# Kernel tuning notes

Hardware: AMD Instinct MI355X
Metric: run time of the kernel (lower is better)

## Reference

```python
import jax, jax.numpy as jnp
import numpy as np

B, S, D_IN, D_OUT, H = 2, 2048, 1024, 1024, 16
HD = D_OUT // H

def setup_inputs() -> dict:
    key = jax.random.key(0)
    ks = jax.random.split(key, 6)
    sc_in = 1.0 / np.sqrt(D_IN)
    sc_out = 1.0 / np.sqrt(D_OUT)
    return {
        "x": jax.random.normal(ks[0], (B, S, D_IN), dtype=jnp.float32),
        "Wq": jax.random.uniform(ks[1], (D_IN, D_OUT), jnp.float32, -sc_in, sc_in),
        "Wk": jax.random.uniform(ks[2], (D_IN, D_OUT), jnp.float32, -sc_in, sc_in),
        "Wv": jax.random.uniform(ks[3], (D_IN, D_OUT), jnp.float32, -sc_in, sc_in),
        "Wo": jax.random.uniform(ks[4], (D_OUT, D_OUT), jnp.float32, -sc_out, sc_out),
        "bo": jax.random.uniform(ks[5], (D_OUT,), jnp.float32, -sc_out, sc_out),
    }

def reference(x, Wq, Wk, Wv, Wo, bo):
    b, s, _ = x.shape
    # QKV projections (no bias), split heads -> [b, h, s, hd]
    q = (x @ Wq).reshape(b, s, H, HD).transpose(0, 2, 1, 3)
    k = (x @ Wk).reshape(b, s, H, HD).transpose(0, 2, 1, 3)
    v = (x @ Wv).reshape(b, s, H, HD).transpose(0, 2, 1, 3)
    scores = jnp.einsum('bhqd,bhkd->bhqk', q, k)
    causal = jnp.triu(jnp.ones((s, s), dtype=bool), k=1)
    scores = jnp.where(causal, -jnp.inf, scores)
    w = jax.nn.softmax(scores / np.sqrt(HD), axis=-1)  # dropout p=0.0 -> identity
    ctx = jnp.einsum('bhqk,bhkd->bhqd', w, v)
    ctx = ctx.transpose(0, 2, 1, 3).reshape(b, s, D_OUT)
    return ctx @ Wo + bo
```

## Files before the change

### kernel.cpp

```cpp
#include <hip/hip_runtime.h>
#include <stdint.h>

typedef unsigned short u16;
typedef __attribute__((ext_vector_type(8))) short short8;
typedef __attribute__((ext_vector_type(4))) float floatx4;
typedef __attribute__((ext_vector_type(4))) u16 ushort4v;

typedef __attribute__((address_space(1))) const uint32_t gu32;
typedef __attribute__((address_space(3))) uint32_t lu32;

#define MFMA(a, b, c) __builtin_amdgcn_mfma_f32_16x16x32_bf16((a), (b), (c), 0, 0, 0)

__device__ __forceinline__ u16 f2bf(float f) {
    union { float f; uint32_t u; } x; x.f = f;
    uint32_t u = x.u;
    u += 0x7fffu + ((u >> 16) & 1u);
    return (u16)(u >> 16);
}

__device__ __forceinline__ void async16(u16* lds, const u16* g) {
    __builtin_amdgcn_global_load_lds((gu32*)g, (lu32*)lds, 16, 0, 0);
}

__global__ __launch_bounds__(256) void prep_kernel(
    const float* __restrict__ x,
    const float* __restrict__ W0, const float* __restrict__ W1,
    const float* __restrict__ W2, const float* __restrict__ W3,
    u16* __restrict__ WT, u16* __restrict__ Xbf)
{
    const int z = blockIdx.z;
    const int tx = threadIdx.x, ty = threadIdx.y;
    if (z == 4) {
        const int bid = blockIdx.y * 32 + blockIdx.x;
        const int t = ty * 32 + tx;
        const size_t base = ((size_t)bid * 256 + t) * 16;
        const float* xf = x + base;
        short8 v0, v1;
#pragma unroll
        for (int j = 0; j < 8; j++) v0[j] = (short)f2bf(xf[j]);
#pragma unroll
        for (int j = 0; j < 8; j++) v1[j] = (short)f2bf(xf[8 + j]);
        *(short8*)&Xbf[base] = v0;
        *(short8*)&Xbf[base + 8] = v1;
        return;
    }
    __shared__ u16 tile[32][33];
    const float* W = (z == 0) ? W0 : (z == 1) ? W1 : (z == 2) ? W2 : W3;
    u16* dst = WT + (size_t)z * 1024 * 1024;
    const int n0 = blockIdx.x * 32, k0 = blockIdx.y * 32;
#pragma unroll
    for (int i = 0; i < 4; i++)
        tile[ty + i * 8][tx] = f2bf(W[(size_t)(k0 + ty + i * 8) * 1024 + n0 + tx]);
    __syncthreads();
#pragma unroll
    for (int i = 0; i < 4; i++)
        dst[(size_t)(n0 + ty + i * 8) * 1024 + k0 + tx] = tile[tx][ty + i * 8];
}

__global__ __launch_bounds__(256) void gemm_qkv_kernel(
    const u16* __restrict__ X, const u16* __restrict__ WT,
    u16* __restrict__ Q, u16* __restrict__ Kout, u16* __restrict__ VT)
{
    __shared__ __align__(16) u16 As[128 * 32];
    __shared__ __align__(16) u16 Bs[128 * 32];
    const int bid = blockIdx.x;
    const int xcd = bid & 7;
    const int idx = bid >> 3;
    const int mat = idx >> 5;
    const int rr  = (idx >> 3) & 3;
    const int nn  = idx & 7;
    const int m0 = (xcd * 4 + rr) * 128;
    const int n0 = nn * 128;
    const u16* BW = WT + (size_t)mat * 1024 * 1024;
    const int tid = threadIdx.x;
    const int wave = tid >> 6, lane = tid & 63;
    const int lrow = lane & 15, lquad = lane >> 4;
    const int wr = (wave >> 1) * 64, wc = (wave & 1) * 64;

    const int ci0 = wave * 128 + lane;
    const int ci1 = ci0 + 64;
    const int ar0 = ci0 >> 2, ac0 = (ci0 & 3) * 8;
    const int ar1 = ci1 >> 2, ac1 = (ci1 & 3) * 8;
    u16* ldsA0 = As + (size_t)(wave * 128) * 8;
    u16* ldsA1 = As + (size_t)(wave * 128 + 64) * 8;
    u16* ldsB0 = Bs + (size_t)(wave * 128) * 8;
    u16* ldsB1 = Bs + (size_t)(wave * 128 + 64) * 8;
    const u16* gA0 = &X[(size_t)(m0 + ar0) * 1024 + ac0];
    const u16* gA1 = &X[(size_t)(m0 + ar1) * 1024 + ac1];
    const u16* gB0 = &BW[(size_t)(n0 + ar0) * 1024 + ac0];
    const u16* gB1 = &BW[(size_t)(n0 + ar1) * 1024 + ac1];

    floatx4 acc[4][4];
#pragma unroll
    for (int mt = 0; mt < 4; mt++)
#pragma unroll
        for (int nt = 0; nt < 4; nt++) acc[mt][nt] = (floatx4){0.f, 0.f, 0.f, 0.f};

    for (int k0 = 0; k0 < 1024; k0 += 32) {
        __syncthreads();
        async16(ldsA0, gA0 + k0);
        async16(ldsA1, gA1 + k0);
        async16(ldsB0, gB0 + k0);
        async16(ldsB1, gB1 + k0);
        __syncthreads();
        short8 af[4], bf[4];
#pragma unroll
        for (int mt = 0; mt < 4; mt++)
            af[mt] = *(const short8*)&As[(wr + mt * 16 + lrow) * 32 + lquad * 8];
#pragma unroll
        for (int nt = 0; nt < 4; nt++)
            bf[nt] = *(const short8*)&Bs[(wc + nt * 16 + lrow) * 32 + lquad * 8];
#pragma unroll
        for (int mt = 0; mt < 4; mt++)
#pragma unroll
            for (int nt = 0; nt < 4; nt++)
                acc[mt][nt] = MFMA(af[mt], bf[nt], acc[mt][nt]);
    }

#pragma unroll
    for (int mt = 0; mt < 4; mt++) {
        const int gm = m0 + wr + mt * 16 + lquad * 4;
        const int b_ = gm >> 11;
        const int s  = gm & 2047;
#pragma unroll
        for (int nt = 0; nt < 4; nt++) {
            const int gn = n0 + wc + nt * 16 + lrow;
            const int h = gn >> 6, hd = gn & 63;
            const int bh = b_ * 16 + h;
            if (mat == 2) {
                ushort4v v;
#pragma unroll
                for (int i = 0; i < 4; i++) v[i] = f2bf(acc[mt][nt][i]);
                *(ushort4v*)&VT[((size_t)bh * 64 + hd) * 2048 + s] = v;
            } else {
                u16* dst = (mat == 0) ? Q : Kout;
#pragma unroll
                for (int i = 0; i < 4; i++)
                    dst[((size_t)bh * 2048 + s + i) * 64 + hd] = f2bf(acc[mt][nt][i]);
            }
        }
    }
}

__global__ __launch_bounds__(256, 4) void attn_kernel(
    const u16* __restrict__ Q, const u16* __restrict__ Kk,
    const u16* __restrict__ VT, u16* __restrict__ ctx)
{
    __shared__ __align__(16) u16 Ks[64][72];
    __shared__ __align__(16) u16 Vs[64][72];
    __shared__ __align__(16) u16 P[4][16][72];
    const int tid = threadIdx.x, wave = tid >> 6, lane = tid & 63;
    const int lrow = lane & 15, lquad = lane >> 4;
    const float scale = 0.125f;
    const float NEGINF = -__builtin_inff();

    const int bh = blockIdx.x & 31;
    const int g = blockIdx.x >> 5;
    const int qb = (g < 16) ? (31 - g) : (g - 16);
    const int ntiles = qb + 1;
    const int q0 = qb * 64 + wave * 16;

    const u16* Qb = Q  + (size_t)bh * 2048 * 64;
    const u16* Kb = Kk + (size_t)bh * 2048 * 64;
    const u16* Vb = VT + (size_t)bh * 64 * 2048;

    const short8 qf0 = *(const short8*)&Qb[(size_t)(q0 + lrow) * 64 + lquad * 8];
    const short8 qf1 = *(const short8*)&Qb[(size_t)(q0 + lrow) * 64 + 32 + lquad * 8];

    const int myq = q0 + lrow;
    float m_s = NEGINF, l_s = 0.f;
    floatx4 o[4];
#pragma unroll
    for (int i = 0; i < 4; i++) o[i] = (floatx4){0.f, 0.f, 0.f, 0.f};

    const int r0 = tid >> 3, c0 = (tid & 7) * 8;
    const int r1 = (tid + 256) >> 3, c1 = c0;

    short8 kreg0 = *(const short8*)&Kb[(size_t)r0 * 64 + c0];
    short8 kreg1 = *(const short8*)&Kb[(size_t)r1 * 64 + c1];
    short8 vreg0 = *(const short8*)&Vb[(size_t)r0 * 2048 + c0];
    short8 vreg1 = *(const short8*)&Vb[(size_t)r1 * 2048 + c1];

    for (int kt = 0; kt < ntiles; kt++) {
        __syncthreads();
        *(short8*)&Ks[r0][c0] = kreg0;
        *(short8*)&Ks[r1][c1] = kreg1;
        *(short8*)&Vs[r0][c0] = vreg0;
        *(short8*)&Vs[r1][c1] = vreg1;
        if (kt + 1 < ntiles) {
            kreg0 = *(const short8*)&Kb[(size_t)((kt + 1) * 64 + r0) * 64 + c0];
            kreg1 = *(const short8*)&Kb[(size_t)((kt + 1) * 64 + r1) * 64 + c1];
            vreg0 = *(const short8*)&Vb[(size_t)r0 * 2048 + (kt + 1) * 64 + c0];
            vreg1 = *(const short8*)&Vb[(size_t)r1 * 2048 + (kt + 1) * 64 + c1];
        }
        __syncthreads();

        floatx4 s[4];
#pragma unroll
        for (int nt = 0; nt < 4; nt++) {
            const short8 kf0 = *(const short8*)&Ks[nt * 16 + lrow][lquad * 8];
            const short8 kf1 = *(const short8*)&Ks[nt * 16 + lrow][32 + lquad * 8];
            floatx4 a = (floatx4){0.f, 0.f, 0.f, 0.f};
            a = MFMA(kf0, qf0, a);
            a = MFMA(kf1, qf1, a);
            s[nt] = a;
        }

        const bool diag = (kt == ntiles - 1);
        float mx = NEGINF;
#pragma unroll
        for (int nt = 0; nt < 4; nt++)
#pragma unroll
            for (int i = 0; i < 4; i++) {
                float v = s[nt][i] * scale;
                if (diag && (kt * 64 + nt * 16 + lquad * 4 + i > myq)) v = NEGINF;
                s[nt][i] = v;
                mx = fmaxf(mx, v);
            }
        mx = fmaxf(mx, __shfl_xor(mx, 16));
        mx = fmaxf(mx, __shfl_xor(mx, 32));
        const float mnew = fmaxf(m_s, mx);
        const float alpha = __expf(m_s - mnew);
        m_s = mnew;
        float sum = 0.f;
#pragma unroll
        for (int nt = 0; nt < 4; nt++)
#pragma unroll
            for (int i = 0; i < 4; i++) {
                const float pv = __expf(s[nt][i] - mnew);
                s[nt][i] = pv;
                sum += pv;
            }
        sum += __shfl_xor(sum, 16);
        sum += __shfl_xor(sum, 32);
        l_s = l_s * alpha + sum;
#pragma unroll
        for (int ht = 0; ht < 4; ht++)
#pragma unroll
            for (int i = 0; i < 4; i++) o[ht][i] *= alpha;

#pragma unroll
        for (int nt = 0; nt < 4; nt++) {
            uint32_t pk0 = (uint32_t)f2bf(s[nt][0]) | ((uint32_t)f2bf(s[nt][1]) << 16);
            uint32_t pk1 = (uint32_t)f2bf(s[nt][2]) | ((uint32_t)f2bf(s[nt][3]) << 16);
            uint2 pk = {pk0, pk1};
            *(uint2*)&P[wave][lrow][nt * 16 + lquad * 4] = pk;
        }
#pragma unroll
        for (int st = 0; st < 2; st++) {
            const short8 pf = *(const short8*)&P[wave][lrow][st * 32 + lquad * 8];
#pragma unroll
            for (int ht = 0; ht < 4; ht++) {
                const short8 vf = *(const short8*)&Vs[ht * 16 + lrow][st * 32 + lquad * 8];
                o[ht] = MFMA(vf, pf, o[ht]);
            }
        }
    }

    const int b_ = bh >> 4, h_ = bh & 15;
    const float inv_l = 1.0f / l_s;
#pragma unroll
    for (int ht = 0; ht < 4; ht++) {
        uint32_t pk0 = (uint32_t)f2bf(o[ht][0] * inv_l) | ((uint32_t)f2bf(o[ht][1] * inv_l) << 16);
        uint32_t pk1 = (uint32_t)f2bf(o[ht][2] * inv_l) | ((uint32_t)f2bf(o[ht][3] * inv_l) << 16);
        uint2 pk = {pk0, pk1};
        *(uint2*)&ctx[((size_t)(b_ * 2048 + q0 + lrow)) * 1024 + h_ * 64 + ht * 16 + lquad * 4] = pk;
    }
}

__global__ __launch_bounds__(256) void gemm_out_kernel(
    const u16* __restrict__ X, const u16* __restrict__ WT,
    const float* __restrict__ bias, float* __restrict__ out)
{
    __shared__ __align__(16) u16 As[128 * 32];
    __shared__ __align__(16) u16 Bs[128 * 32];
    const int bid = blockIdx.x;
    const int xcd = bid & 7;
    const int idx = bid >> 3;
    const int rr  = idx >> 3;
    const int nn  = idx & 7;
    const int m0 = (xcd * 4 + rr) * 128;
    const int n0 = nn * 128;
    const int tid = threadIdx.x;
    const int wave = tid >> 6, lane = tid & 63;
    const int lrow = lane & 15, lquad = lane >> 4;
    const int wr = (wave >> 1) * 64, wc = (wave & 1) * 64;

    const int ci0 = wave * 128 + lane;
    const int ci1 = ci0 + 64;
    const int ar0 = ci0 >> 2, ac0 = (ci0 & 3) * 8;
    const int ar1 = ci1 >> 2, ac1 = (ci1 & 3) * 8;
    u16* ldsA0 = As + (size_t)(wave * 128) * 8;
    u16* ldsA1 = As + (size_t)(wave * 128 + 64) * 8;
    u16* ldsB0 = Bs + (size_t)(wave * 128) * 8;
    u16* ldsB1 = Bs + (size_t)(wave * 128 + 64) * 8;
    const u16* gA0 = &X[(size_t)(m0 + ar0) * 1024 + ac0];
    const u16* gA1 = &X[(size_t)(m0 + ar1) * 1024 + ac1];
    const u16* gB0 = &WT[(size_t)(n0 + ar0) * 1024 + ac0];
    const u16* gB1 = &WT[(size_t)(n0 + ar1) * 1024 + ac1];

    floatx4 acc[4][4];
#pragma unroll
    for (int mt = 0; mt < 4; mt++)
#pragma unroll
        for (int nt = 0; nt < 4; nt++) acc[mt][nt] = (floatx4){0.f, 0.f, 0.f, 0.f};

    for (int k0 = 0; k0 < 1024; k0 += 32) {
        __syncthreads();
        async16(ldsA0, gA0 + k0);
        async16(ldsA1, gA1 + k0);
        async16(ldsB0, gB0 + k0);
        async16(ldsB1, gB1 + k0);
        __syncthreads();
        short8 af[4], bf[4];
#pragma unroll
        for (int mt = 0; mt < 4; mt++)
            af[mt] = *(const short8*)&As[(wr + mt * 16 + lrow) * 32 + lquad * 8];
#pragma unroll
        for (int nt = 0; nt < 4; nt++)
            bf[nt] = *(const short8*)&Bs[(wc + nt * 16 + lrow) * 32 + lquad * 8];
#pragma unroll
        for (int mt = 0; mt < 4; mt++)
#pragma unroll
            for (int nt = 0; nt < 4; nt++)
                acc[mt][nt] = MFMA(af[mt], bf[nt], acc[mt][nt]);
    }

#pragma unroll
    for (int mt = 0; mt < 4; mt++) {
        const int gm = m0 + wr + mt * 16 + lquad * 4;
#pragma unroll
        for (int nt = 0; nt < 4; nt++) {
            const int gn = n0 + wc + nt * 16 + lrow;
            const float bv = bias[gn];
#pragma unroll
            for (int i = 0; i < 4; i++)
                out[(size_t)(gm + i) * 1024 + gn] = acc[mt][nt][i] + bv;
        }
    }
}

extern "C" void kernel_launch(void* const* d_in, const int* in_sizes, int n_in,
                              void* d_out, int out_size, void* d_ws, size_t ws_size,
                              hipStream_t stream) {
    u16* ws = (u16*)d_ws + 64;

    const size_t MB1 = 1024 * 1024;
    u16* WT   = ws;
    u16* Qw   = ws + 4 * MB1;
    u16* Kw   = ws + 8 * MB1;
    u16* VTw  = ws + 12 * MB1;
    u16* ctxw = ws + 16 * MB1;
    u16* Xbf  = ws + 20 * MB1;

    prep_kernel<<<dim3(32, 32, 5), dim3(32, 8), 0, stream>>>(
        (const float*)d_in[0], (const float*)d_in[1], (const float*)d_in[2],
        (const float*)d_in[3], (const float*)d_in[4], WT, Xbf);
    gemm_qkv_kernel<<<768, 256, 0, stream>>>(Xbf, WT, Qw, Kw, VTw);
    attn_kernel<<<1024, 256, 0, stream>>>(Qw, Kw, VTw, ctxw);
    gemm_out_kernel<<<256, 256, 0, stream>>>(ctxw, WT + 3 * MB1, (const float*)d_in[5], (float*)d_out);
}
```

Baseline: 181.6 us.

## Double-buffer K/V via async LDS loads with swizzled tile layout and exp2 softmax

The QKV GEMM epilogue now writes K and V in per-64-row tiles with an XOR swizzle, so the attention kernel can copy each tile straight into LDS with global_load_lds. K/V tiles are double-buffered, which removes the register staging and one barrier per iteration. Q is pre-scaled by scale*log2e so the softmax can use exp2 without a per-element multiply. P is packed to bf16 by truncation. The risks are correctness of the async-load waits under a single barrier, and the slightly different rounding of P.

```diff
diff --git a/kernel.cpp b/kernel.cpp
--- a/kernel.cpp
+++ b/kernel.cpp
@@ -10,12 +10,18 @@
 typedef __attribute__((address_space(3))) uint32_t lu32;
 
 #define MFMA(a, b, c) __builtin_amdgcn_mfma_f32_16x16x32_bf16((a), (b), (c), 0, 0, 0)
+
+#define QSCALE 0.1803368801111204f
 
 __device__ __forceinline__ u16 f2bf(float f) {
     union { float f; uint32_t u; } x; x.f = f;
     uint32_t u = x.u;
     u += 0x7fffu + ((u >> 16) & 1u);
     return (u16)(u >> 16);
+}
+
+__device__ __forceinline__ uint32_t pack_trunc(float hi, float lo) {
+    return __builtin_amdgcn_perm(__float_as_uint(hi), __float_as_uint(lo), 0x07060302u);
 }
 
 __device__ __forceinline__ void async16(u16* lds, const u16* g) {
@@ -122,36 +128,45 @@
         const int gm = m0 + wr + mt * 16 + lquad * 4;
         const int b_ = gm >> 11;
         const int s  = gm & 2047;
+        const int kt = s >> 6;
+        const int r  = s & 63;
 #pragma unroll
         for (int nt = 0; nt < 4; nt++) {
             const int gn = n0 + wc + nt * 16 + lrow;
             const int h = gn >> 6, hd = gn & 63;
             const int bh = b_ * 16 + h;
             if (mat == 2) {
+                const size_t base = ((size_t)(bh * 32 + kt) * 64 + hd) * 64
+                                  + ((((r >> 3) ^ (hd & 7)) << 3) | (r & 7));
                 ushort4v v;
 #pragma unroll
                 for (int i = 0; i < 4; i++) v[i] = f2bf(acc[mt][nt][i]);
-                *(ushort4v*)&VT[((size_t)bh * 64 + hd) * 2048 + s] = v;
+                *(ushort4v*)&VT[base] = v;
+            } else if (mat == 1) {
+#pragma unroll
+                for (int i = 0; i < 4; i++) {
+                    const int r2 = r + i;
+                    Kout[((size_t)(bh * 32 + kt) * 64 + r2) * 64
+                         + (((hd >> 3) ^ (r2 & 7)) << 3) + (hd & 7)] = f2bf(acc[mt][nt][i]);
+                }
             } else {
-                u16* dst = (mat == 0) ? Q : Kout;
 #pragma unroll
                 for (int i = 0; i < 4; i++)
-                    dst[((size_t)bh * 2048 + s + i) * 64 + hd] = f2bf(acc[mt][nt][i]);
+                    Q[((size_t)bh * 2048 + s + i) * 64 + hd] = f2bf(acc[mt][nt][i] * QSCALE);
             }
         }
     }
 }
 
 __global__ __launch_bounds__(256, 4) void attn_kernel(
-    const u16* __restrict__ Q, const u16* __restrict__ Kk,
-    const u16* __restrict__ VT, u16* __restrict__ ctx)
+    const u16* __restrict__ Q, const u16* __restrict__ Ksw,
+    const u16* __restrict__ Vsw, u16* __restrict__ ctx)
 {
-    __shared__ __align__(16) u16 Ks[64][72];
-    __shared__ __align__(16) u16 Vs[64][72];
-    __shared__ __align__(16) u16 P[4][16][72];
+    __shared__ __align__(16) u16 Ks[2][4096];
+    __shared__ __align__(16) u16 Vs[2][4096];
+    __shared__ __align__(16) u16 P[4][1024];
     const int tid = threadIdx.x, wave = tid >> 6, lane = tid & 63;
     const int lrow = lane & 15, lquad = lane >> 4;
-    const float scale = 0.125f;
     const float NEGINF = -__builtin_inff();
 
     const int bh = blockIdx.x & 31;
@@ -160,12 +175,35 @@
     const int ntiles = qb + 1;
     const int q0 = qb * 64 + wave * 16;
 
-    const u16* Qb = Q  + (size_t)bh * 2048 * 64;
-    const u16* Kb = Kk + (size_t)bh * 2048 * 64;
-    const u16* Vb = VT + (size_t)bh * 64 * 2048;
+    const u16* Qb = Q   + (size_t)bh * 2048 * 64;
+    const u16* Kt = Ksw + (size_t)bh * 32 * 4096;
+    const u16* Vt = Vsw + (size_t)bh * 32 * 4096;
 
     const short8 qf0 = *(const short8*)&Qb[(size_t)(q0 + lrow) * 64 + lquad * 8];
     const short8 qf1 = *(const short8*)&Qb[(size_t)(q0 + lrow) * 64 + 32 + lquad * 8];
+
+    const int r7 = lrow & 7;
+    int koff0[4], koff1[4], voff[2][4];
+#pragma unroll
+    for (int nt = 0; nt < 4; nt++) {
+        const int row = nt * 16 + lrow;
+        koff0[nt] = row * 64 + ((lquad ^ r7) << 3);
+        koff1[nt] = row * 64 + (((4 + lquad) ^ r7) << 3);
+    }
+#pragma unroll
+    for (int st = 0; st < 2; st++)
+#pragma unroll
+        for (int ht = 0; ht < 4; ht++) {
+            const int row = ht * 16 + lrow;
+            voff[st][ht] = row * 64 + (((st * 4 + lquad) ^ r7) << 3);
+        }
+    int pwoff[4], proff[2];
+#pragma unroll
+    for (int nt = 0; nt < 4; nt++)
+        pwoff[nt] = lrow * 64 + (((nt * 2 + (lquad >> 1)) ^ r7) << 3) + ((lquad & 1) << 2);
+#pragma unroll
+    for (int st = 0; st < 2; st++)
+        proff[st] = lrow * 64 + (((st * 4 + lquad) ^ r7) << 3);
 
     const int myq = q0 + lrow;
     float m_s = NEGINF, l_s = 0.f;
@@ -173,33 +211,36 @@
 #pragma unroll
     for (int i = 0; i < 4; i++) o[i] = (floatx4){0.f, 0.f, 0.f, 0.f};
 
-    const int r0 = tid >> 3, c0 = (tid & 7) * 8;
-    const int r1 = (tid + 256) >> 3, c1 = c0;
-
-    short8 kreg0 = *(const short8*)&Kb[(size_t)r0 * 64 + c0];
-    short8 kreg1 = *(const short8*)&Kb[(size_t)r1 * 64 + c1];
-    short8 vreg0 = *(const short8*)&Vb[(size_t)r0 * 2048 + c0];
-    short8 vreg1 = *(const short8*)&Vb[(size_t)r1 * 2048 + c1];
+    const int co0 = wave * 1024;
+    const int co1 = wave * 1024 + 512;
+    const int lo8 = lane * 8;
+
+    async16(&Ks[0][co0], Kt + co0 + lo8);
+    async16(&Ks[0][co1], Kt + co1 + lo8);
+    async16(&Vs[0][co0], Vt + co0 + lo8);
+    async16(&Vs[0][co1], Vt + co1 + lo8);
+
+    u16* Pw = P[wave];
 
     for (int kt = 0; kt < ntiles; kt++) {
         __syncthreads();
-        *(short8*)&Ks[r0][c0] = kreg0;
-        *(short8*)&Ks[r1][c1] = kreg1;
-        *(short8*)&Vs[r0][c0] = vreg0;
-        *(short8*)&Vs[r1][c1] = vreg1;
         if (kt + 1 < ntiles) {
-            kreg0 = *(const short8*)&Kb[(size_t)((kt + 1) * 64 + r0) * 64 + c0];
-            kreg1 = *(const short8*)&Kb[(size_t)((kt + 1) * 64 + r1) * 64 + c1];
-            vreg0 = *(const short8*)&Vb[(size_t)r0 * 2048 + (kt + 1) * 64 + c0];
-            vreg1 = *(const short8*)&Vb[(size_t)r1 * 2048 + (kt + 1) * 64 + c1];
-        }
-        __syncthreads();
+            const u16* Kn = Kt + (size_t)(kt + 1) * 4096;
+            const u16* Vn = Vt + (size_t)(kt + 1) * 4096;
+            const int nb = (kt + 1) & 1;
+            async16(&Ks[nb][co0], Kn + co0 + lo8);
+            async16(&Ks[nb][co1], Kn + co1 + lo8);
+            async16(&Vs[nb][co0], Vn + co0 + lo8);
+            async16(&Vs[nb][co1], Vn + co1 + lo8);
+        }
+        const u16* kbuf = Ks[kt & 1];
+        const u16* vbuf = Vs[kt & 1];
 
         floatx4 s[4];
 #pragma unroll
         for (int nt = 0; nt < 4; nt++) {
-            const short8 kf0 = *(const short8*)&Ks[nt * 16 + lrow][lquad * 8];
-            const short8 kf1 = *(const short8*)&Ks[nt * 16 + lrow][32 + lquad * 8];
+            const short8 kf0 = *(const short8*)&kbuf[koff0[nt]];
+            const short8 kf1 = *(const short8*)&kbuf[koff1[nt]];
             floatx4 a = (floatx4){0.f, 0.f, 0.f, 0.f};
             a = MFMA(kf0, qf0, a);
             a = MFMA(kf1, qf1, a);
@@ -207,27 +248,29 @@
         }
 
         const bool diag = (kt == ntiles - 1);
+        if (diag) {
+#pragma unroll
+            for (int nt = 0; nt < 4; nt++)
+#pragma unroll
+                for (int i = 0; i < 4; i++)
+                    if (kt * 64 + nt * 16 + lquad * 4 + i > myq) s[nt][i] = NEGINF;
+        }
         float mx = NEGINF;
 #pragma unroll
         for (int nt = 0; nt < 4; nt++)
 #pragma unroll
-            for (int i = 0; i < 4; i++) {
-                float v = s[nt][i] * scale;
-                if (diag && (kt * 64 + nt * 16 + lquad * 4 + i > myq)) v = NEGINF;
-                s[nt][i] = v;
-                mx = fmaxf(mx, v);
-            }
+            for (int i = 0; i < 4; i++) mx = fmaxf(mx, s[nt][i]);
         mx = fmaxf(mx, __shfl_xor(mx, 16));
         mx = fmaxf(mx, __shfl_xor(mx, 32));
         const float mnew = fmaxf(m_s, mx);
-        const float alpha = __expf(m_s - mnew);
+        const float alpha = exp2f(m_s - mnew);
         m_s = mnew;
         float sum = 0.f;
 #pragma unroll
         for (int nt = 0; nt < 4; nt++)
 #pragma unroll
             for (int i = 0; i < 4; i++) {
-                const float pv = __expf(s[nt][i] - mnew);
+                const float pv = exp2f(s[nt][i] - mnew);
                 s[nt][i] = pv;
                 sum += pv;
             }
@@ -241,17 +284,17 @@
 
 #pragma unroll
         for (int nt = 0; nt < 4; nt++) {
-            uint32_t pk0 = (uint32_t)f2bf(s[nt][0]) | ((uint32_t)f2bf(s[nt][1]) << 16);
-            uint32_t pk1 = (uint32_t)f2bf(s[nt][2]) | ((uint32_t)f2bf(s[nt][3]) << 16);
-            uint2 pk = {pk0, pk1};
-            *(uint2*)&P[wave][lrow][nt * 16 + lquad * 4] = pk;
+            uint2 pk;
+            pk.x = pack_trunc(s[nt][1], s[nt][0]);
+            pk.y = pack_trunc(s[nt][3], s[nt][2]);
+            *(uint2*)&Pw[pwoff[nt]] = pk;
         }
 #pragma unroll
         for (int st = 0; st < 2; st++) {
-            const short8 pf = *(const short8*)&P[wave][lrow][st * 32 + lquad * 8];
+            const short8 pf = *(const short8*)&Pw[proff[st]];
 #pragma unroll
             for (int ht = 0; ht < 4; ht++) {
-                const short8 vf = *(const short8*)&Vs[ht * 16 + lrow][st * 32 + lquad * 8];
+                const short8 vf = *(const short8*)&vbuf[voff[st][ht]];
                 o[ht] = MFMA(vf, pf, o[ht]);
             }
         }
```

Measured after the change: 197.8 us. 1.09x slower.
